# Optimization experiments

Hardware: AMD Instinct MI355X
Metric: run time of the kernel (lower is better)

## Reference

```python
import jax, jax.numpy as jnp
import numpy as np

N = 256          # num_nodes per graph
B = 64           # batch_size (len(data.y))
NLAY = 3
F_IN = 5
NE = N * N       # num_edges per graph
NN = B * N       # total nodes
TEMP = 0.6
ALPHA = 0.1      # propagation residual alpha
BB_ALPHA = 0.8   # BBEdge_pred alpha
K = 2


def setup_inputs() -> dict:
    key = jax.random.key(0)
    ks = jax.random.split(key, 8)
    n_tril = N * (N + 1) // 2
    x = jax.random.normal(ks[0], (NN, F_IN), jnp.float32)
    # lower-triangular (incl. diagonal) entries of the learned adjacency
    edge_weight_param = jax.random.normal(ks[1], (n_tril,), jnp.float32)
    # BBEdge_pred params per layer (torch init: U(1.0,1.5), U(0.49,0.51))
    a_uc = 1.0 + 0.5 * jax.random.uniform(ks[2], (NLAY,), jnp.float32)
    b_uc = 0.49 + 0.02 * jax.random.uniform(ks[3], (NLAY,), jnp.float32)
    # randomness for Kumaraswamy pi sample and RelaxedBernoulli rsample
    u_pi = jax.random.uniform(ks[4], (NLAY,), jnp.float32)
    u_rb = jax.random.uniform(ks[5], (NLAY, NE), jnp.float32)
    lin_w = jax.random.normal(ks[6], (F_IN, 128), jnp.float32) / np.float32(np.sqrt(F_IN))
    lin_b = jnp.zeros((128,), jnp.float32)
    fc_w = jax.random.normal(ks[7], (128, 3), jnp.float32) / np.float32(np.sqrt(128))
    fc_b = jnp.zeros((3,), jnp.float32)
    # dense block-diagonal edge_index: graph b owns nodes [b*N, (b+1)*N); edge k=i*N+j -> (i,j)
    base = jnp.arange(N, dtype=jnp.int32)
    rows = jnp.repeat(base, N)
    cols = jnp.tile(base, N)
    offs = (jnp.arange(B, dtype=jnp.int32) * N)[:, None]
    edge_index = jnp.stack([(offs + rows[None, :]).reshape(-1),
                            (offs + cols[None, :]).reshape(-1)])
    batch = jnp.repeat(jnp.arange(B, dtype=jnp.int32), N)
    return {"x": x, "edge_weight_param": edge_weight_param, "a_uc": a_uc, "b_uc": b_uc,
            "u_pi": u_pi, "u_rb": u_rb, "lin_w": lin_w, "lin_b": lin_b,
            "fc_w": fc_w, "fc_b": fc_b, "edge_index": edge_index, "batch": batch}


def _forward(x, edge_weight_param, a_uc, b_uc, u_pi, u_rb,
             lin_w, lin_b, fc_w, fc_b, edge_index, batch):
    row, col = edge_index[0], edge_index[1]
    # symmetrized dense edge-weight matrix from tril params
    xs, ys = jnp.tril_indices(N)
    W = jnp.zeros((N, N), x.dtype).at[xs, ys].set(edge_weight_param)
    W = W + W.T - jnp.diag(jnp.diag(W))
    w_full = jnp.tile(W.reshape(-1), B)                      # [E]
    # GCN-style degree normalization (self-loops already on diagonal)
    deg = jax.ops.segment_sum(jnp.abs(w_full), row, num_segments=NN)
    dis = jnp.where(deg > 0, deg ** -0.5, 0.0)
    adj = dis[row] * w_full * dis[col]                       # [E]

    # Beta-Bernoulli edge keep-prob and RelaxedBernoulli masks
    a = jax.nn.softplus(jnp.clip(a_uc, -10.0, None))
    b = jax.nn.softplus(jnp.clip(b_uc, -10.0, 50.0))
    up = jnp.clip(u_pi, 1e-6, 1.0 - 1e-6)
    pi = (1.0 - up ** (1.0 / b)) ** (1.0 / a)                # [NLAY]
    ur = jnp.clip(u_rb, 1e-6, 1.0 - 1e-6)
    logits = jnp.log(pi) - jnp.log1p(-pi)                    # [NLAY]
    z = jax.nn.sigmoid((logits[:, None] + jnp.log(ur) - jnp.log1p(-ur)) / TEMP)  # [NLAY, NE]

    def conv(xx, w_e):
        # emb = alpha*x + (1-alpha)/K * scatter(col, w_e * x[row])
        msg = w_e[:, None] * xx[row]                          # [E, F]
        agg = jax.ops.segment_sum(msg, col, num_segments=NN)
        return ALPHA * xx + (1.0 - ALPHA) / K * agg

    emb = ALPHA * x
    # layer 0: masked adjacency
    x1 = conv(x, jnp.tile(z[0], B) * adj)
    emb = emb + (1.0 - ALPHA) * x1 / NLAY
    # layer 1 (middle): unmasked conv, then masked block conv (nblock=1, fp=5)
    x2 = conv(x1, adj)
    emb = emb + (1.0 - ALPHA) * x2 / NLAY
    x3 = jax.nn.relu(conv(x2[:, :F_IN], jnp.tile(z[1], B) * adj))  # dropout off (eval)
    # layer 2 (last)
    x4 = conv(x3, adj)
    emb = emb + (1.0 - ALPHA) * x4 / NLAY
    o = conv(x4, jnp.tile(z[2], B) * adj)
    out = jax.nn.relu(o @ lin_w + lin_b)                      # [NN, 128]

    # KL regularizer summed over layers
    euler = 0.577215664901532
    kld = ((1.0 - BB_ALPHA / a) * (-euler - jax.scipy.special.digamma(b) - 1.0 / b)
           + jnp.log(a * b + 1e-10) - jnp.log(jnp.float32(BB_ALPHA)) - (b - 1.0) / b)
    kld_loss = jnp.sum(kld)

    pooled = jax.ops.segment_sum(out, batch, num_segments=B)  # global_add_pool -> [B, 128]
    output = pooled @ fc_w + fc_b                             # [B, 3]
    drop_rates = pi[:, None]                                  # [NLAY, 1]
    return output, kld_loss, drop_rates


def reference(x, edge_weight_param, a_uc, b_uc, u_pi, u_rb,
              lin_w, lin_b, fc_w, fc_b, edge_index, batch):
    return _forward(x, edge_weight_param, a_uc, b_uc, u_pi, u_rb,
                    lin_w, lin_b, fc_w, fc_b, edge_index, batch)
```

## Files before the change

kernel.cpp:

```cpp
#include <hip/hip_runtime.h>
#include <math.h>

#define NN_ 256
#define BB_ 64
#define FF_ 5
#define NE_ 65536

#define OFF_SLA 0
#define OFF_SL1 65536
#define OFF_SL3 131072
#define OFF_SL5 196608
#define OFF_DIS 262144

__global__ __launch_bounds__(256) void build_all(
    const float* __restrict__ p, const float* __restrict__ u_rb,
    const float* __restrict__ a_uc, const float* __restrict__ b_uc,
    const float* __restrict__ u_pi, float* __restrict__ ws,
    float* __restrict__ out) {
  const int i = blockIdx.x, j = threadIdx.x;
  const int t = (i >= j) ? (i * (i + 1) / 2 + j) : (j * (j + 1) / 2 + i);
  const float w = p[t];

  __shared__ float sh[NN_];
  __shared__ float slg[3];
  __shared__ float skld[3];
  sh[j] = fabsf(w);

  if (j < 3) {
    const int l = j;
    const float au = fmaxf(a_uc[l], -10.0f);
    const float bu = fminf(fmaxf(b_uc[l], -10.0f), 50.0f);
    const float a = log1pf(expf(au));
    const float b = log1pf(expf(bu));
    const float up = fminf(fmaxf(u_pi[l], 1e-6f), 1.0f - 1e-6f);
    const float pi = powf(1.0f - powf(up, 1.0f / b), 1.0f / a);
    slg[l] = logf(pi) - log1pf(-pi);
    if (i == 0) {
      out[193 + l] = pi;
      float x = b, dg = 0.0f;
      while (x < 6.0f) { dg -= 1.0f / x; x += 1.0f; }
      const float inv = 1.0f / x, inv2 = inv * inv;
      dg += logf(x) - 0.5f * inv
            - inv2 * (1.0f / 12.0f - inv2 * (1.0f / 120.0f - inv2 * (1.0f / 252.0f)));
      const float euler = 0.577215664901532f;
      skld[l] = (1.0f - 0.8f / a) * (-euler - dg - 1.0f / b)
                + logf(a * b + 1e-10f) - logf(0.8f) - (b - 1.0f) / b;
    }
  }
  __syncthreads();

  for (int s = NN_ / 2; s > 0; s >>= 1) {
    if (j < s) sh[j] += sh[j + s];
    __syncthreads();
  }
  if (j == 0) {
    const float deg = sh[0];
    ws[OFF_DIS + i] = (deg > 0.0f) ? (1.0f / sqrtf(deg)) : 0.0f;
    if (i == 0) out[192] = skld[0] + skld[1] + skld[2];
  }

  const float lg0 = slg[0];
  const float lg1 = slg[1];
  const float lg2 = slg[2];
  const int idx = i * NN_ + j;
  const float inv_temp = 1.0f / 0.6f;

  ws[OFF_SLA + idx] = w;

  float u, v;
  u = fminf(fmaxf(u_rb[0 * NE_ + idx], 1e-6f), 1.0f - 1e-6f);
  v = (lg0 + logf(u) - log1pf(-u)) * inv_temp;
  ws[OFF_SL1 + idx] = w / (1.0f + expf(-v));

  u = fminf(fmaxf(u_rb[1 * NE_ + idx], 1e-6f), 1.0f - 1e-6f);
  v = (lg1 + logf(u) - log1pf(-u)) * inv_temp;
  ws[OFF_SL3 + idx] = w / (1.0f + expf(-v));

  u = fminf(fmaxf(u_rb[2 * NE_ + idx], 1e-6f), 1.0f - 1e-6f);
  v = (lg2 + logf(u) - log1pf(-u)) * inv_temp;
  ws[OFF_SL5 + idx] = w / (1.0f + expf(-v));
}

__global__ __launch_bounds__(1024) void batch_chain(
    const float* __restrict__ x0g, const float* __restrict__ ws,
    const float* __restrict__ lin_w, const float* __restrict__ lin_b,
    const float* __restrict__ fc_w, const float* __restrict__ fc_b,
    float* __restrict__ out) {
  const int b = blockIdx.x, tid = threadIdx.x;
  __shared__ float xbuf[2][NN_ * 8];
  __shared__ float sbuf[2][NN_ * 8];
  __shared__ float part[8 * NN_ * 8];
  __shared__ float sdis[NN_];
  float* Xc = xbuf[0];
  float* Xn = xbuf[1];
  float* Sc = sbuf[0];
  float* Sn = sbuf[1];

  for (int ii = tid; ii < NN_; ii += 1024) sdis[ii] = ws[OFF_DIS + ii];
  for (int idx = tid; idx < NN_ * FF_; idx += 1024) {
    const int i = idx / 5, f = idx - 5 * i;
    Xc[i * 8 + f] = x0g[b * (NN_ * FF_) + idx];
  }
  __syncthreads();
  for (int idx = tid; idx < 2048; idx += 1024)
    Sc[idx] = sdis[idx >> 3] * Xc[idx];
  __syncthreads();

  const int q = tid >> 7;
  const int j0 = tid & 127;
  const int k0 = q * 32;

#pragma unroll
  for (int l = 0; l < 5; ++l) {
    const float* __restrict__ Op =
        ws + (l == 0 ? OFF_SL1 : l == 2 ? OFF_SL3 : l == 4 ? OFF_SL5 : OFF_SLA)
        + j0;
    float4 p03 = {0.f, 0.f, 0.f, 0.f};
    float4 r03 = {0.f, 0.f, 0.f, 0.f};
    float p4 = 0.f, r4 = 0.f;
#pragma unroll 8
    for (int k = k0; k < k0 + 32; ++k) {
      const float w0 = Op[k * NN_];
      const float w1 = Op[k * NN_ + 128];
      const float4 xv = *(const float4*)(Sc + k * 8);
      const float x4 = Sc[k * 8 + 4];
      p03.x += w0 * xv.x; p03.y += w0 * xv.y;
      p03.z += w0 * xv.z; p03.w += w0 * xv.w; p4 += w0 * x4;
      r03.x += w1 * xv.x; r03.y += w1 * xv.y;
      r03.z += w1 * xv.z; r03.w += w1 * xv.w; r4 += w1 * x4;
    }
    float* const pp0 = part + (q * NN_ + j0) * 8;
    float* const pp1 = part + (q * NN_ + j0 + 128) * 8;
    *(float4*)pp0 = p03; pp0[4] = p4;
    *(float4*)pp1 = r03; pp1[4] = r4;
    __syncthreads();
    for (int idx = tid; idx < 2048; idx += 1024) {
      float sum = part[idx];
#pragma unroll
      for (int qq = 1; qq < 8; ++qq) sum += part[qq * 2048 + idx];
      const float dj = sdis[idx >> 3];
      float y = 0.1f * Xc[idx] + 0.45f * dj * sum;
      if (l == 2) y = fmaxf(y, 0.f);
      Xn[idx] = y;
      Sn[idx] = dj * y;
    }
    __syncthreads();
    float* tp = Xc; Xc = Xn; Xn = tp;
    tp = Sc; Sc = Sn; Sn = tp;
  }

  const int k = tid & 127, seg = tid >> 7;
  const float lw0 = lin_w[0 * 128 + k];
  const float lw1 = lin_w[1 * 128 + k];
  const float lw2 = lin_w[2 * 128 + k];
  const float lw3 = lin_w[3 * 128 + k];
  const float lw4 = lin_w[4 * 128 + k];
  const float lb = lin_b[k];
  float acc = 0.f;
  const int r0 = seg * 32;
#pragma unroll 4
  for (int jj = r0; jj < r0 + 32; ++jj) {
    const float4 ov = *(const float4*)(Xc + jj * 8);
    const float o4 = Xc[jj * 8 + 4];
    const float vv = lb + lw0 * ov.x + lw1 * ov.y + lw2 * ov.z +
                     lw3 * ov.w + lw4 * o4;
    acc += fmaxf(vv, 0.f);
  }
  part[seg * 128 + k] = acc;
  __syncthreads();
  if (tid < 128) {
    float s = 0.f;
#pragma unroll
    for (int s8 = 0; s8 < 8; ++s8) s += part[s8 * 128 + tid];
    part[tid] = s;
  }
  __syncthreads();
  if (tid < 3) {
    float s = fc_b[tid];
    for (int kk = 0; kk < 128; ++kk) s += part[kk] * fc_w[kk * 3 + tid];
    out[b * 3 + tid] = s;
  }
}

extern "C" void kernel_launch(void* const* d_in, const int* in_sizes, int n_in,
                              void* d_out, int out_size, void* d_ws,
                              size_t ws_size, hipStream_t stream) {
  const float* x      = (const float*)d_in[0];
  const float* p      = (const float*)d_in[1];
  const float* a_uc   = (const float*)d_in[2];
  const float* b_uc   = (const float*)d_in[3];
  const float* u_pi   = (const float*)d_in[4];
  const float* u_rb   = (const float*)d_in[5];
  const float* lin_w  = (const float*)d_in[6];
  const float* lin_b  = (const float*)d_in[7];
  const float* fc_w   = (const float*)d_in[8];
  const float* fc_b   = (const float*)d_in[9];
  float* out = (float*)d_out;
  float* ws  = (float*)d_ws;

  build_all<<<256, 256, 0, stream>>>(p, u_rb, a_uc, b_uc, u_pi, ws, out);
  batch_chain<<<64, 1024, 0, stream>>>(x, ws, lin_w, lin_b, fc_w, fc_b, out);
}
```

Baseline: 126.5 us.

## Precompose linear propagation operators into two dense matrices before batched chain

Each propagation step becomes a full normalized operator (0.1·I + 0.45·D·S·D). The linear runs between ReLUs are premultiplied into two 256x256 matrices, one for layers 1-3 and one for layers 4-5, using small GEMM kernels. The per-graph chain then does two matrix-vector passes instead of five and no longer needs the degree-scaling buffers. In exchange it adds three extra kernel launches and three N^3 GEMMs shared across the batch, and float32 associativity changes slightly alter rounding.

```diff
diff --git a/kernel.cpp b/kernel.cpp
--- a/kernel.cpp
+++ b/kernel.cpp
@@ -11,6 +11,13 @@
 #define OFF_SL3 131072
 #define OFF_SL5 196608
 #define OFF_DIS 262144
+#define OFF_FA  327680
+#define OFF_FZ0 393216
+#define OFF_FZ1 458752
+#define OFF_FZ2 524288
+#define OFF_T1  589824
+#define OFF_MTA 655360
+#define OFF_MTB 720896
 
 __global__ __launch_bounds__(256) void build_all(
     const float* __restrict__ p, const float* __restrict__ u_rb,
@@ -81,6 +88,67 @@
   ws[OFF_SL5 + idx] = w / (1.0f + expf(-v));
 }
 
+__global__ __launch_bounds__(256) void norm_ops(float* __restrict__ ws) {
+  const int i = blockIdx.x, j = threadIdx.x;
+  const int idx = i * NN_ + j;
+  const float di = ws[OFF_DIS + i];
+  const float dj = ws[OFF_DIS + j];
+  const float s = 0.45f * di * dj;
+  const float d = (i == j) ? 0.1f : 0.0f;
+  ws[OFF_FA  + idx] = d + s * ws[OFF_SLA + idx];
+  ws[OFF_FZ0 + idx] = d + s * ws[OFF_SL1 + idx];
+  ws[OFF_FZ1 + idx] = d + s * ws[OFF_SL3 + idx];
+  ws[OFF_FZ2 + idx] = d + s * ws[OFF_SL5 + idx];
+}
+
+__global__ __launch_bounds__(256) void gemm_pair(float* __restrict__ ws) {
+  const int bid = blockIdx.x, j = threadIdx.x;
+  const int r = bid & 255;
+  const bool g2 = bid >= 256;
+  const float* __restrict__ F = ws + (g2 ? OFF_FA : OFF_FZ0) + r * NN_;
+  const float* __restrict__ G = ws + (g2 ? OFF_FZ2 : OFF_FA) + j;
+  float* __restrict__ D = ws + (g2 ? OFF_MTB : OFF_T1) + r * NN_ + j;
+
+  __shared__ float Fr[NN_];
+  Fr[j] = F[j];
+  __syncthreads();
+
+  float a0 = 0.f, a1 = 0.f, a2 = 0.f, a3 = 0.f;
+#pragma unroll 4
+  for (int k = 0; k < NN_; k += 4) {
+    a0 += Fr[k + 0] * G[(k + 0) * NN_];
+    a1 += Fr[k + 1] * G[(k + 1) * NN_];
+    a2 += Fr[k + 2] * G[(k + 2) * NN_];
+    a3 += Fr[k + 3] * G[(k + 3) * NN_];
+  }
+  *D = (a0 + a1) + (a2 + a3);
+}
+
+__global__ __launch_bounds__(512) void gemm_mta(float* __restrict__ ws) {
+  const int r = blockIdx.x;
+  const int tid = threadIdx.x;
+  const int j = tid & 255, h = tid >> 8;
+  __shared__ float Tr[NN_];
+  __shared__ float prt[2][NN_];
+  if (tid < NN_) Tr[tid] = ws[OFF_T1 + r * NN_ + tid];
+  __syncthreads();
+
+  const float* __restrict__ G = ws + OFF_FZ1 + j;
+  const int k0 = h * 128;
+  float a0 = 0.f, a1 = 0.f, a2 = 0.f, a3 = 0.f;
+#pragma unroll 4
+  for (int k = k0; k < k0 + 128; k += 4) {
+    a0 += Tr[k + 0] * G[(k + 0) * NN_];
+    a1 += Tr[k + 1] * G[(k + 1) * NN_];
+    a2 += Tr[k + 2] * G[(k + 2) * NN_];
+    a3 += Tr[k + 3] * G[(k + 3) * NN_];
+  }
+  prt[h][j] = (a0 + a1) + (a2 + a3);
+  __syncthreads();
+  if (tid < NN_)
+    ws[OFF_MTA + r * NN_ + tid] = prt[0][tid] + prt[1][tid];
+}
+
 __global__ __launch_bounds__(1024) void batch_chain(
     const float* __restrict__ x0g, const float* __restrict__ ws,
     const float* __restrict__ lin_w, const float* __restrict__ lin_b,
@@ -88,33 +156,23 @@
     float* __restrict__ out) {
   const int b = blockIdx.x, tid = threadIdx.x;
   __shared__ float xbuf[2][NN_ * 8];
-  __shared__ float sbuf[2][NN_ * 8];
   __shared__ float part[8 * NN_ * 8];
-  __shared__ float sdis[NN_];
   float* Xc = xbuf[0];
   float* Xn = xbuf[1];
-  float* Sc = sbuf[0];
-  float* Sn = sbuf[1];
-
-  for (int ii = tid; ii < NN_; ii += 1024) sdis[ii] = ws[OFF_DIS + ii];
+
   for (int idx = tid; idx < NN_ * FF_; idx += 1024) {
     const int i = idx / 5, f = idx - 5 * i;
     Xc[i * 8 + f] = x0g[b * (NN_ * FF_) + idx];
   }
   __syncthreads();
-  for (int idx = tid; idx < 2048; idx += 1024)
-    Sc[idx] = sdis[idx >> 3] * Xc[idx];
-  __syncthreads();
 
   const int q = tid >> 7;
   const int j0 = tid & 127;
   const int k0 = q * 32;
 
 #pragma unroll
-  for (int l = 0; l < 5; ++l) {
-    const float* __restrict__ Op =
-        ws + (l == 0 ? OFF_SL1 : l == 2 ? OFF_SL3 : l == 4 ? OFF_SL5 : OFF_SLA)
-        + j0;
+  for (int l = 0; l < 2; ++l) {
+    const float* __restrict__ Op = ws + (l == 0 ? OFF_MTA : OFF_MTB) + j0;
     float4 p03 = {0.f, 0.f, 0.f, 0.f};
     float4 r03 = {0.f, 0.f, 0.f, 0.f};
     float p4 = 0.f, r4 = 0.f;
@@ -122,8 +180,8 @@
     for (int k = k0; k < k0 + 32; ++k) {
       const float w0 = Op[k * NN_];
       const float w1 = Op[k * NN_ + 128];
-      const float4 xv = *(const float4*)(Sc + k * 8);
-      const float x4 = Sc[k * 8 + 4];
+      const float4 xv = *(const float4*)(Xc + k * 8);
+      const float x4 = Xc[k * 8 + 4];
       p03.x += w0 * xv.x; p03.y += w0 * xv.y;
       p03.z += w0 * xv.z; p03.w += w0 * xv.w; p4 += w0 * x4;
       r03.x += w1 * xv.x; r03.y += w1 * xv.y;
@@ -138,15 +196,10 @@
       float sum = part[idx];
 #pragma unroll
       for (int qq = 1; qq < 8; ++qq) sum += part[qq * 2048 + idx];
-      const float dj = sdis[idx >> 3];
-      float y = 0.1f * Xc[idx] + 0.45f * dj * sum;
-      if (l == 2) y = fmaxf(y, 0.f);
-      Xn[idx] = y;
-      Sn[idx] = dj * y;
+      Xn[idx] = (l == 0) ? fmaxf(sum, 0.f) : sum;
     }
     __syncthreads();
     float* tp = Xc; Xc = Xn; Xn = tp;
-    tp = Sc; Sc = Sn; Sn = tp;
   }
 
   const int k = tid & 127, seg = tid >> 7;
@@ -199,5 +252,8 @@
   float* ws  = (float*)d_ws;
 
   build_all<<<256, 256, 0, stream>>>(p, u_rb, a_uc, b_uc, u_pi, ws, out);
+  norm_ops<<<256, 256, 0, stream>>>(ws);
+  gemm_pair<<<512, 256, 0, stream>>>(ws);
+  gemm_mta<<<256, 512, 0, stream>>>(ws);
   batch_chain<<<64, 1024, 0, stream>>>(x, ws, lin_w, lin_b, fc_w, fc_b, out);
 }
```

Result: slower. 131.7 us (+4.1%).

## Precompose linear propagation operators into two dense matrices before batch chain

Applied to the files above, without the earlier changes.

Folds the degree normalization and residual terms into dense 256x256 operator matrices, then multiplies them once with two new GEMM kernels. The per-batch chain then runs two matrix applications instead of five, with a ReLU after the first. This removes per-graph repeated work across 64 blocks. In exchange it adds two kernel launches and about 3 extra 256^3 products, and reassociation changes floating-point rounding.

```diff
diff --git a/kernel.cpp b/kernel.cpp
--- a/kernel.cpp
+++ b/kernel.cpp
@@ -11,6 +11,9 @@
 #define OFF_SL3 131072
 #define OFF_SL5 196608
 #define OFF_DIS 262144
+#define OFF_T2  327680
+#define OFF_MTA 393216
+#define OFF_MTB 458752
 
 __global__ __launch_bounds__(256) void build_all(
     const float* __restrict__ p, const float* __restrict__ u_rb,
@@ -53,9 +56,10 @@
     if (j < s) sh[j] += sh[j + s];
     __syncthreads();
   }
+  const float deg = sh[0];
+  const float disi = (deg > 0.0f) ? (1.0f / sqrtf(deg)) : 0.0f;
   if (j == 0) {
-    const float deg = sh[0];
-    ws[OFF_DIS + i] = (deg > 0.0f) ? (1.0f / sqrtf(deg)) : 0.0f;
+    ws[OFF_DIS + i] = disi;
     if (i == 0) out[192] = skld[0] + skld[1] + skld[2];
   }
 
@@ -64,21 +68,97 @@
   const float lg2 = slg[2];
   const int idx = i * NN_ + j;
   const float inv_temp = 1.0f / 0.6f;
-
-  ws[OFF_SLA + idx] = w;
+  const float wd = w * disi;
+
+  ws[OFF_SLA + idx] = wd;
 
   float u, v;
   u = fminf(fmaxf(u_rb[0 * NE_ + idx], 1e-6f), 1.0f - 1e-6f);
   v = (lg0 + logf(u) - log1pf(-u)) * inv_temp;
-  ws[OFF_SL1 + idx] = w / (1.0f + expf(-v));
+  ws[OFF_SL1 + idx] = wd / (1.0f + expf(-v));
 
   u = fminf(fmaxf(u_rb[1 * NE_ + idx], 1e-6f), 1.0f - 1e-6f);
   v = (lg1 + logf(u) - log1pf(-u)) * inv_temp;
-  ws[OFF_SL3 + idx] = w / (1.0f + expf(-v));
+  ws[OFF_SL3 + idx] = wd / (1.0f + expf(-v));
 
   u = fminf(fmaxf(u_rb[2 * NE_ + idx], 1e-6f), 1.0f - 1e-6f);
   v = (lg2 + logf(u) - log1pf(-u)) * inv_temp;
-  ws[OFF_SL5 + idx] = w / (1.0f + expf(-v));
+  ws[OFF_SL5 + idx] = wd / (1.0f + expf(-v));
+}
+
+__global__ __launch_bounds__(1024) void gemm_round1(float* __restrict__ ws) {
+  const int bid = blockIdx.x;
+  const int r = bid & 255;
+  const bool g2 = bid >= 256;
+  const int tid = threadIdx.x;
+  const int j = tid & 255, kq = tid >> 8;
+
+  __shared__ float Fr[NN_];
+  __shared__ float sdis[NN_];
+  __shared__ float part[4][NN_];
+
+  if (tid < NN_) sdis[tid] = ws[OFF_DIS + tid];
+  __syncthreads();
+  if (tid < NN_) {
+    float v = 0.45f * ws[OFF_SLA + r * NN_ + tid] * sdis[tid];
+    if (tid == r) v += 0.1f;
+    Fr[tid] = v;
+  }
+  __syncthreads();
+
+  const float cj = 0.45f * sdis[j];
+  const float* __restrict__ Gp = ws + (g2 ? OFF_SL5 : OFF_SL3) + j;
+  const int k0 = kq * 64;
+  float a0 = 0.f, a1 = 0.f, a2 = 0.f, a3 = 0.f;
+#pragma unroll 4
+  for (int k = k0; k < k0 + 64; k += 4) {
+    float g0 = cj * Gp[(k + 0) * NN_]; if (k + 0 == j) g0 += 0.1f;
+    float g1 = cj * Gp[(k + 1) * NN_]; if (k + 1 == j) g1 += 0.1f;
+    float g2v = cj * Gp[(k + 2) * NN_]; if (k + 2 == j) g2v += 0.1f;
+    float g3 = cj * Gp[(k + 3) * NN_]; if (k + 3 == j) g3 += 0.1f;
+    a0 += Fr[k + 0] * g0;
+    a1 += Fr[k + 1] * g1;
+    a2 += Fr[k + 2] * g2v;
+    a3 += Fr[k + 3] * g3;
+  }
+  part[kq][j] = (a0 + a1) + (a2 + a3);
+  __syncthreads();
+  if (tid < NN_)
+    ws[(g2 ? OFF_MTB : OFF_T2) + r * NN_ + tid] =
+        (part[0][tid] + part[1][tid]) + (part[2][tid] + part[3][tid]);
+}
+
+__global__ __launch_bounds__(1024) void gemm_round2(float* __restrict__ ws) {
+  const int r = blockIdx.x;
+  const int tid = threadIdx.x;
+  const int j = tid & 255, kq = tid >> 8;
+
+  __shared__ float Fr[NN_];
+  __shared__ float part[4][NN_];
+
+  if (tid < NN_) {
+    const float dk = ws[OFF_DIS + tid];
+    float v = 0.45f * ws[OFF_SL1 + r * NN_ + tid] * dk;
+    if (tid == r) v += 0.1f;
+    Fr[tid] = v;
+  }
+  __syncthreads();
+
+  const float* __restrict__ Gp = ws + OFF_T2 + j;
+  const int k0 = kq * 64;
+  float a0 = 0.f, a1 = 0.f, a2 = 0.f, a3 = 0.f;
+#pragma unroll 4
+  for (int k = k0; k < k0 + 64; k += 4) {
+    a0 += Fr[k + 0] * Gp[(k + 0) * NN_];
+    a1 += Fr[k + 1] * Gp[(k + 1) * NN_];
+    a2 += Fr[k + 2] * Gp[(k + 2) * NN_];
+    a3 += Fr[k + 3] * Gp[(k + 3) * NN_];
+  }
+  part[kq][j] = (a0 + a1) + (a2 + a3);
+  __syncthreads();
+  if (tid < NN_)
+    ws[OFF_MTA + r * NN_ + tid] =
+        (part[0][tid] + part[1][tid]) + (part[2][tid] + part[3][tid]);
 }
 
 __global__ __launch_bounds__(1024) void batch_chain(
@@ -88,33 +168,23 @@
     float* __restrict__ out) {
   const int b = blockIdx.x, tid = threadIdx.x;
   __shared__ float xbuf[2][NN_ * 8];
-  __shared__ float sbuf[2][NN_ * 8];
   __shared__ float part[8 * NN_ * 8];
-  __shared__ float sdis[NN_];
   float* Xc = xbuf[0];
   float* Xn = xbuf[1];
-  float* Sc = sbuf[0];
-  float* Sn = sbuf[1];
-
-  for (int ii = tid; ii < NN_; ii += 1024) sdis[ii] = ws[OFF_DIS + ii];
+
   for (int idx = tid; idx < NN_ * FF_; idx += 1024) {
     const int i = idx / 5, f = idx - 5 * i;
     Xc[i * 8 + f] = x0g[b * (NN_ * FF_) + idx];
   }
   __syncthreads();
-  for (int idx = tid; idx < 2048; idx += 1024)
-    Sc[idx] = sdis[idx >> 3] * Xc[idx];
-  __syncthreads();
 
   const int q = tid >> 7;
   const int j0 = tid & 127;
   const int k0 = q * 32;
 
 #pragma unroll
-  for (int l = 0; l < 5; ++l) {
-    const float* __restrict__ Op =
-        ws + (l == 0 ? OFF_SL1 : l == 2 ? OFF_SL3 : l == 4 ? OFF_SL5 : OFF_SLA)
-        + j0;
+  for (int l = 0; l < 2; ++l) {
+    const float* __restrict__ Op = ws + (l == 0 ? OFF_MTA : OFF_MTB) + j0;
     float4 p03 = {0.f, 0.f, 0.f, 0.f};
     float4 r03 = {0.f, 0.f, 0.f, 0.f};
     float p4 = 0.f, r4 = 0.f;
@@ -122,8 +192,8 @@
     for (int k = k0; k < k0 + 32; ++k) {
       const float w0 = Op[k * NN_];
       const float w1 = Op[k * NN_ + 128];
-      const float4 xv = *(const float4*)(Sc + k * 8);
-      const float x4 = Sc[k * 8 + 4];
+      const float4 xv = *(const float4*)(Xc + k * 8);
+      const float x4 = Xc[k * 8 + 4];
       p03.x += w0 * xv.x; p03.y += w0 * xv.y;
       p03.z += w0 * xv.z; p03.w += w0 * xv.w; p4 += w0 * x4;
       r03.x += w1 * xv.x; r03.y += w1 * xv.y;
@@ -138,15 +208,10 @@
       float sum = part[idx];
 #pragma unroll
       for (int qq = 1; qq < 8; ++qq) sum += part[qq * 2048 + idx];
-      const float dj = sdis[idx >> 3];
-      float y = 0.1f * Xc[idx] + 0.45f * dj * sum;
-      if (l == 2) y = fmaxf(y, 0.f);
-      Xn[idx] = y;
-      Sn[idx] = dj * y;
+      Xn[idx] = (l == 0) ? fmaxf(sum, 0.f) : sum;
     }
     __syncthreads();
     float* tp = Xc; Xc = Xn; Xn = tp;
-    tp = Sc; Sc = Sn; Sn = tp;
   }
 
   const int k = tid & 127, seg = tid >> 7;
@@ -199,5 +264,7 @@
   float* ws  = (float*)d_ws;
 
   build_all<<<256, 256, 0, stream>>>(p, u_rb, a_uc, b_uc, u_pi, ws, out);
+  gemm_round1<<<512, 1024, 0, stream>>>(ws);
+  gemm_round2<<<256, 1024, 0, stream>>>(ws);
   batch_chain<<<64, 1024, 0, stream>>>(x, ws, lin_w, lin_b, fc_w, fc_b, out);
 }
```

New measurement: 130.4 us. +3.1%, slower.
